# Kernel optimization log

Hardware: AMD Instinct MI355X
Metric: run time of the kernel (lower is better)

## Reference

```python
import math
import jax, jax.numpy as jnp
import numpy as np

B, S, H = 2, 2048, 1024
NH = 16
HD = H // NH            # 64
ROT = int(HD * 0.25)    # 16
QKV_SLOTS = 1024
PROJ_SLOTS = 1024
FFN_SLOTS = 4096
EPS = 1e-5


def gelu_l2_norm(x, axis=-1):
    # F.gelu (exact erf) then L2-normalize and rescale by sqrt(dim)
    g = jax.nn.gelu(x, approximate=False)
    n = jnp.linalg.norm(g, ord=2, axis=axis, keepdims=True)
    return g / n * math.sqrt(g.shape[axis])


def layer_norm(x, w, b):
    mu = jnp.mean(x, axis=-1, keepdims=True)
    var = jnp.mean(jnp.square(x - mu), axis=-1, keepdims=True)
    return (x - mu) * jax.lax.rsqrt(var + EPS) * w + b


def pattention(x, key_tok, val_tok):
    # [.., in] @ [slots, in]^T -> [.., slots]; NOTE: scale MULTIPLIES (as in source)
    aw = jnp.einsum('bsh,ph->bsp', x, key_tok) * math.sqrt(x.shape[-1])
    aw = gelu_l2_norm(aw, axis=-1)
    return jnp.einsum('bsp,pd->bsd', aw, val_tok)


def rotary_cos_sin(seq_len, rot_dim, base=10000.0):
    inv_freq = 1.0 / (base ** (jnp.arange(0, rot_dim, 2, dtype=jnp.float32) / rot_dim))
    t = jnp.arange(seq_len, dtype=jnp.float32)
    freqs = jnp.einsum('s,d->sd', t, inv_freq)           # [S, rot/2]
    emb = jnp.concatenate([freqs, freqs], axis=-1)       # [S, rot]
    return jnp.cos(emb), jnp.sin(emb)


def rotate_half(x):
    x1, x2 = jnp.split(x, 2, axis=-1)
    return jnp.concatenate([-x2, x1], axis=-1)


def setup_inputs() -> dict:
    key = jax.random.key(0)
    ks = jax.random.split(key, 12)
    p = lambda k, shape: jax.random.normal(k, shape, dtype=jnp.float32) * 0.02
    return {
        'x': jax.random.normal(ks[0], (B, S, H), dtype=jnp.float32),
        'ln1_w': jnp.ones((H,), jnp.float32), 'ln1_b': jnp.zeros((H,), jnp.float32),
        'ln2_w': jnp.ones((H,), jnp.float32), 'ln2_b': jnp.zeros((H,), jnp.float32),
        'q_key': p(ks[1], (QKV_SLOTS, H)), 'q_val': p(ks[2], (QKV_SLOTS, H)),
        'k_key': p(ks[3], (QKV_SLOTS, H)), 'k_val': p(ks[4], (QKV_SLOTS, H)),
        'v_key': p(ks[5], (QKV_SLOTS, H)), 'v_val': p(ks[6], (QKV_SLOTS, H)),
        'proj_key': p(ks[7], (PROJ_SLOTS, H)), 'proj_val': p(ks[8], (PROJ_SLOTS, H)),
        'ffn_key': p(ks[9], (FFN_SLOTS, H)), 'ffn_val': p(ks[10], (FFN_SLOTS, H)),
    }


def reference(x, ln1_w, ln1_b, ln2_w, ln2_b, q_key, q_val, k_key, k_val,
              v_key, v_val, proj_key, proj_val, ffn_key, ffn_val):
    residual = x
    xn = layer_norm(x, ln1_w, ln1_b)
    q = pattention(xn, q_key, q_val).reshape(B, S, NH, HD)
    k = pattention(xn, k_key, k_val).reshape(B, S, NH, HD)
    v = pattention(xn, v_key, v_val).reshape(B, S, NH, HD)

    cos, sin = rotary_cos_sin(S, ROT)          # [S, ROT]
    cos = cos[None, :, None, :]
    sin = sin[None, :, None, :]
    q_rot, q_pass = q[..., :ROT], q[..., ROT:]
    k_rot, k_pass = k[..., :ROT], k[..., ROT:]
    q_rot = q_rot * cos + rotate_half(q_rot) * sin
    k_rot = k_rot * cos + rotate_half(k_rot) * sin
    q = jnp.concatenate([q_rot, q_pass], axis=-1).transpose(0, 2, 1, 3)  # [B,NH,S,HD]
    k = jnp.concatenate([k_rot, k_pass], axis=-1).transpose(0, 2, 1, 3)
    v = v.transpose(0, 2, 1, 3)

    scale = math.sqrt(HD)
    causal = jnp.triu(jnp.ones((S, S), dtype=bool), k=1)
    attn_mask = jnp.where(causal, jnp.float32(-10000.0), jnp.float32(0.0))
    aw = jnp.einsum('bhqd,bhkd->bhqk', q, k) / scale + attn_mask
    aw = gelu_l2_norm(aw, axis=-1)
    o = jnp.einsum('bhqk,bhkd->bhqd', aw, v)
    o = o.transpose(0, 2, 1, 3).reshape(B, S, H)

    x = residual + pattention(o, proj_key, proj_val)
    residual = x
    x = residual + pattention(layer_norm(x, ln2_w, ln2_b), ffn_key, ffn_val)
    return x
```

## Files before the change

### kernel.cpp

```cpp
#include <hip/hip_runtime.h>

typedef __bf16 bf16x8 __attribute__((ext_vector_type(8)));
typedef float f32x4 __attribute__((ext_vector_type(4)));
typedef unsigned short u16;

__device__ __forceinline__ float b2f(u16 u) {
  union { unsigned int i; float f; } v; v.i = ((unsigned int)u) << 16; return v.f;
}
__device__ __forceinline__ u16 f2b(float f) {
  union { float f; unsigned int i; } v; v.f = f;
  unsigned int x = v.i;
  x += 0x7fffu + ((x >> 16) & 1u);
  return (u16)(x >> 16);
}
__device__ __forceinline__ float gelu_f(float x) {
  float x2 = x * x;
  float p = x * (1.5957691216f + 0.0713548162f * x2);
  float e = __expf(p);
  float r = __builtin_amdgcn_rcpf(1.0f + e);
  return x - x * r;
}
__device__ __forceinline__ void async16(const u16* g, u16* l) {
  __builtin_amdgcn_global_load_lds(
      (const __attribute__((address_space(1))) void*)g,
      (__attribute__((address_space(3))) void*)l, 16, 0, 0);
}
__device__ __forceinline__ void swz(int& bn, int& bm, int& bz) {
  int gx = (int)gridDim.x, gy = (int)gridDim.y;
  int flat = (int)(blockIdx.x + gridDim.x * (blockIdx.y + gridDim.y * blockIdx.z));
  int seq = flat >> 3;
  int nbm = gy >> 3;
  bm = (flat & 7) * nbm + seq % nbm;
  int rest = seq / nbm;
  bn = rest % gx;
  bz = rest / gx;
}

union U4 { uint4 u; u16 s[8]; };

__global__ __launch_bounds__(256) void cvt9_kernel(
    const float* __restrict__ qk, const float* __restrict__ kk,
    const float* __restrict__ vk, const float* __restrict__ pk,
    const float* __restrict__ fk, u16* __restrict__ w, float* __restrict__ ssqz) {
  int z = blockIdx.y;
  int i = blockIdx.x * 256 + threadIdx.x;
  if (z == 8) {
    if (i < 20480) ssqz[i] = 0.f;
    return;
  }
  const float* in = (z == 0) ? qk : (z == 1) ? kk : (z == 2) ? vk : (z == 3) ? pk
                    : fk + (size_t)(z - 4) * 1048576;
  u16* o = w + (size_t)z * 1048576;
  float4 f = ((const float4*)in)[i];
  ushort4 s;
  s.x = f2b(f.x); s.y = f2b(f.y); s.z = f2b(f.z); s.w = f2b(f.w);
  ((ushort4*)o)[i] = s;
}

__global__ __launch_bounds__(256) void cvtT8_kernel(
    const float* __restrict__ qv, const float* __restrict__ kv,
    const float* __restrict__ vv, const float* __restrict__ pv,
    const float* __restrict__ fv, u16* __restrict__ valsT, u16* __restrict__ fvT) {
  __shared__ float t[32][33];
  int z = blockIdx.z;
  const float* in; u16* o; int Rout, rowoff;
  if (z < 4) {
    in = (z == 0) ? qv : (z == 1) ? kv : (z == 2) ? vv : pv;
    o = valsT + (size_t)z * 1048576; Rout = 1024; rowoff = 0;
  } else {
    in = fv + (size_t)(z - 4) * 1048576;
    o = fvT; Rout = 4096; rowoff = (z - 4) * 1024;
  }
  int bc = blockIdx.x, br = blockIdx.y;
  int tid = threadIdx.x;
  int r = tid >> 5, cc = tid & 31;
  #pragma unroll
  for (int i = 0; i < 4; ++i)
    t[r + i * 8][cc] = in[(size_t)(br * 32 + r + i * 8) * 1024 + bc * 32 + cc];
  __syncthreads();
  #pragma unroll
  for (int i = 0; i < 4; ++i)
    o[(size_t)(bc * 32 + r + i * 8) * Rout + rowoff + br * 32 + cc] = f2b(t[cc][r + i * 8]);
}

__global__ __launch_bounds__(256) void ln_kernel(const float* __restrict__ x,
    const float* __restrict__ w, const float* __restrict__ b, u16* __restrict__ out) {
  int wv = threadIdx.x >> 6, lane = threadIdx.x & 63;
  int row = blockIdx.x * 4 + wv;
  const float* xr = x + (size_t)row * 1024;
  float4 v[4];
  float s = 0.f, s2 = 0.f;
  #pragma unroll
  for (int i = 0; i < 4; ++i) {
    v[i] = ((const float4*)xr)[lane + 64 * i];
    s += v[i].x + v[i].y + v[i].z + v[i].w;
    s2 += v[i].x * v[i].x + v[i].y * v[i].y + v[i].z * v[i].z + v[i].w * v[i].w;
  }
  #pragma unroll
  for (int m = 1; m < 64; m <<= 1) { s += __shfl_xor(s, m); s2 += __shfl_xor(s2, m); }
  float mu = s * (1.0f / 1024.0f);
  float inv = rsqrtf(s2 * (1.0f / 1024.0f) - mu * mu + 1e-5f);
  u16* orow = out + (size_t)row * 1024;
  #pragma unroll
  for (int i = 0; i < 4; ++i) {
    int c = (lane + 64 * i) * 4;
    ushort4 o;
    o.x = f2b((v[i].x - mu) * inv * w[c]     + b[c]);
    o.y = f2b((v[i].y - mu) * inv * w[c + 1] + b[c + 1]);
    o.z = f2b((v[i].z - mu) * inv * w[c + 2] + b[c + 2]);
    o.w = f2b((v[i].w - mu) * inv * w[c + 3] + b[c + 3]);
    ((ushort4*)orow)[lane + 64 * i] = o;
  }
}

__device__ __forceinline__ bf16x8 ldfrag(const u16* __restrict__ base, int row, int ks, int quad) {
  int off = (row * 64 + ks * 32 + quad * 8) ^ ((row & 7) << 3);
  return *(const bf16x8*)&base[off];
}

template <int EPI, bool ROT>
__global__ __launch_bounds__(512, 2) void gemm8(
    const u16* __restrict__ A, size_t sAz,
    const u16* __restrict__ B, size_t sBz,
    u16* __restrict__ C, size_t sCz,
    float* __restrict__ ssqb, size_t sSz,
    int N, int K, int kzs, int klen, float alpha) {
  __shared__ __align__(16) u16 As[2][2][8192];
  __shared__ __align__(16) u16 Bs[2][2][8192];
  int bn, bm, bz;
  swz(bn, bm, bz);
  int tid = threadIdx.x, lane = tid & 63, wv = tid >> 6;
  int quad = lane >> 4, l16 = lane & 15;
  int wm = wv >> 2, wn = wv & 3;
  const u16* Ab = A + (size_t)bz * sAz + (size_t)(bm * 256) * K;
  const u16* Bb = B + (size_t)bz * sBz + (size_t)(bn * 256) * K;
  int koff = bz * kzs;
  size_t off0, off1;
  {
    int r0 = wv * 16 + (lane >> 3);
    int r1 = r0 + 8;
    off0 = (size_t)r0 * K + ((lane & 7) ^ (r0 & 7)) * 8;
    off1 = (size_t)r1 * K + ((lane & 7) ^ (r1 & 7)) * 8;
  }
  int lds0 = wv * 1024, lds1 = wv * 1024 + 512;
  const size_t hK = (size_t)128 * K;
  auto STAGE = [&](const u16* gb, int k0, u16* lds) {
    async16(gb + off0 + k0, lds + lds0);
    async16(gb + off1 + k0, lds + lds1);
  };

  f32x4 zero = {0.f, 0.f, 0.f, 0.f};
  f32x4 acc[8][4];
  #pragma unroll
  for (int i = 0; i < 8; ++i)
    #pragma unroll
    for (int j = 0; j < 4; ++j) acc[i][j] = zero;

  int NT = klen >> 6;
  STAGE(Bb,      koff,      &Bs[0][0][0]);
  STAGE(Bb + hK, koff,      &Bs[0][1][0]);
  STAGE(Ab,      koff,      &As[0][0][0]);
  STAGE(Ab + hK, koff,      &As[0][1][0]);
  STAGE(Bb,      koff + 64, &Bs[1][0][0]);
  STAGE(Bb + hK, koff + 64, &Bs[1][1][0]);
  STAGE(Ab,      koff + 64, &As[1][0][0]);
  asm volatile("s_waitcnt vmcnt(6)" ::: "memory");
  __builtin_amdgcn_sched_barrier(0);
  __builtin_amdgcn_s_barrier();

  bf16x8 a[4][2], b[4][2];
  int brow = (wn & 1) * 64;
  for (int t = 0; t < NT; ++t) {
    int cur = t & 1;
    const u16* Ar = &As[cur][wm][0];
    const u16* Br = &Bs[cur][wn >> 1][0];
    #pragma unroll
    for (int j = 0; j < 4; ++j)
      #pragma unroll
      for (int ks = 0; ks < 2; ++ks)
        b[j][ks] = ldfrag(Br, brow + j * 16 + l16, ks, quad);
    #pragma unroll
    for (int i = 0; i < 4; ++i)
      #pragma unroll
      for (int ks = 0; ks < 2; ++ks)
        a[i][ks] = ldfrag(Ar, i * 16 + l16, ks, quad);
    if (t + 1 < NT) STAGE(Ab + hK, koff + (t + 1) * 64, &As[cur ^ 1][1][0]);
    __builtin_amdgcn_s_barrier();
    asm volatile("s_waitcnt lgkmcnt(0)" ::: "memory");
    __builtin_amdgcn_sched_barrier(0);
    __builtin_amdgcn_s_setprio(1);
    #pragma unroll
    for (int i = 0; i < 4; ++i)
      #pragma unroll
      for (int j = 0; j < 2; ++j) {
        acc[i][j] = __builtin_amdgcn_mfma_f32_16x16x32_bf16(a[i][0], b[j][0], acc[i][j], 0, 0, 0);
        acc[i][j] = __builtin_amdgcn_mfma_f32_16x16x32_bf16(a[i][1], b[j][1], acc[i][j], 0, 0, 0);
      }
    __builtin_amdgcn_s_setprio(0);
    __builtin_amdgcn_sched_barrier(0);
    __builtin_amdgcn_s_barrier();
    if (t + 2 < NT) STAGE(Bb, koff + (t + 2) * 64, &Bs[cur][0][0]);
    __builtin_amdgcn_s_barrier();
    __builtin_amdgcn_s_setprio(1);
    #pragma unroll
    for (int i = 0; i < 4; ++i)
      #pragma unroll
      for (int j = 2; j < 4; ++j) {
        acc[i][j] = __builtin_amdgcn_mfma_f32_16x16x32_bf16(a[i][0], b[j][0], acc[i][j], 0, 0, 0);
        acc[i][j] = __builtin_amdgcn_mfma_f32_16x16x32_bf16(a[i][1], b[j][1], acc[i][j], 0, 0, 0);
      }
    __builtin_amdgcn_s_setprio(0);
    __builtin_amdgcn_sched_barrier(0);
    __builtin_amdgcn_s_barrier();
    #pragma unroll
    for (int i = 0; i < 4; ++i)
      #pragma unroll
      for (int ks = 0; ks < 2; ++ks)
        a[i][ks] = ldfrag(Ar, 64 + i * 16 + l16, ks, quad);
    if (t + 2 < NT) STAGE(Bb + hK, koff + (t + 2) * 64, &Bs[cur][1][0]);
    __builtin_amdgcn_s_barrier();
    asm volatile("s_waitcnt lgkmcnt(0)" ::: "memory");
    __builtin_amdgcn_sched_barrier(0);
    __builtin_amdgcn_s_setprio(1);
    #pragma unroll
    for (int i = 0; i < 4; ++i)
      #pragma unroll
      for (int j = 0; j < 2; ++j) {
        acc[4 + i][j] = __builtin_amdgcn_mfma_f32_16x16x32_bf16(a[i][0], b[j][0], acc[4 + i][j], 0, 0, 0);
        acc[4 + i][j] = __builtin_amdgcn_mfma_f32_16x16x32_bf16(a[i][1], b[j][1], acc[4 + i][j], 0, 0, 0);
      }
    __builtin_amdgcn_s_setprio(0);
    __builtin_amdgcn_sched_barrier(0);
    __builtin_amdgcn_s_barrier();
    if (t + 2 < NT) STAGE(Ab, koff + (t + 2) * 64, &As[cur][0][0]);
    __builtin_amdgcn_s_barrier();
    __builtin_amdgcn_s_setprio(1);
    #pragma unroll
    for (int i = 0; i < 4; ++i)
      #pragma unroll
      for (int j = 2; j < 4; ++j) {
        acc[4 + i][j] = __builtin_amdgcn_mfma_f32_16x16x32_bf16(a[i][0], b[j][0], acc[4 + i][j], 0, 0, 0);
        acc[4 + i][j] = __builtin_amdgcn_mfma_f32_16x16x32_bf16(a[i][1], b[j][1], acc[4 + i][j], 0, 0, 0);
      }
    __builtin_amdgcn_s_setprio(0);
    if (t < NT - 1) {
      if (t == NT - 2) asm volatile("s_waitcnt vmcnt(0)" ::: "memory");
      else             asm volatile("s_waitcnt vmcnt(6)" ::: "memory");
    }
    __builtin_amdgcn_sched_barrier(0);
    __builtin_amdgcn_s_barrier();
  }

  #pragma unroll
  for (int i = 0; i < 8; ++i) {
    int rbase = bm * 256 + wm * 128 + i * 16 + quad * 4;
    if (EPI == 0) {
      float srow[4] = {0.f, 0.f, 0.f, 0.f};
      #pragma unroll
      for (int j = 0; j < 4; ++j) {
        int c = bn * 256 + wn * 64 + j * 16 + l16;
        #pragma unroll
        for (int reg = 0; reg < 4; ++reg) {
          float g = gelu_f(acc[i][j][reg] * alpha);
          srow[reg] += g * g;
          C[(size_t)bz * sCz + (size_t)(rbase + reg) * N + c] = f2b(g);
        }
      }
      #pragma unroll
      for (int reg = 0; reg < 4; ++reg) {
        float s = srow[reg];
        s += __shfl_xor(s, 1); s += __shfl_xor(s, 2);
        s += __shfl_xor(s, 4); s += __shfl_xor(s, 8);
        if (l16 == 0) atomicAdd(&ssqb[bz * sSz + rbase + reg], s);
      }
    } else if (EPI == 1) {
      float sc[4];
      #pragma unroll
      for (int reg = 0; reg < 4; ++reg)
        sc[reg] = alpha * rsqrtf(ssqb[bz * sSz + rbase + reg]);
      #pragma unroll
      for (int j = 0; j < 4; ++j) {
        int c = bn * 256 + wn * 64 + j * 16 + l16;
        #pragma unroll
        for (int reg = 0; reg < 4; ++reg) {
          float vs = acc[i][j][reg] * sc[reg];
          if (ROT && j == 0) {
            float prt = __shfl_xor(vs, 8);
            if (bz < 2) {
              int seq = (rbase + reg) & 2047;
              float fr = exp2f((float)(l16 & 7) * -1.66096404744368f);
              float ang = (float)seq * fr;
              float c_ = __cosf(ang), s_ = __sinf(ang);
              vs = (l16 < 8) ? (vs * c_ - prt * s_) : (vs * c_ + prt * s_);
            }
          }
          C[(size_t)bz * sCz + (size_t)(rbase + reg) * N + c] = f2b(vs);
        }
      }
    } else {
      float* Cf = (float*)C + (size_t)(bz >> 1) * sCz;
      #pragma unroll
      for (int j = 0; j < 4; ++j) {
        int c = bn * 256 + wn * 64 + j * 16 + l16;
        #pragma unroll
        for (int reg = 0; reg < 4; ++reg)
          atomicAdd(&Cf[(size_t)(rbase + reg) * N + c], acc[i][j][reg]);
      }
    }
  }
}

__global__ __launch_bounds__(256) void zz_kernel(float* __restrict__ p0,
                                                 float* __restrict__ p1) {
  size_t i = ((size_t)blockIdx.x * 256 + threadIdx.x) * 4;
  float4 z = {0.f, 0.f, 0.f, 0.f};
  *(float4*)(p0 + i) = z;
  *(float4*)(p1 + i) = z;
}

template <int TM>
__global__ __launch_bounds__(256) void gemm_key(
    const u16* __restrict__ A, size_t sAz,
    const u16* __restrict__ B, size_t sBz,
    u16* __restrict__ C, size_t sCz,
    float* __restrict__ ssqb, size_t sSz,
    int N, int K, float alpha) {
  constexpr int AI = TM / 32;
  __shared__ __align__(16) u16 As[2][TM * 32];
  __shared__ __align__(16) u16 Bs[2][128 * 32];
  int bn, bm, bz;
  swz(bn, bm, bz);
  const u16* Ab = A + (size_t)bz * sAz + (size_t)bm * TM * K;
  const u16* Bb = B + (size_t)bz * sBz + (size_t)bn * 128 * K;
  int tid = threadIdx.x, lane = tid & 63, wv = tid >> 6;
  int quad = lane >> 4, l16 = lane & 15;
  int lr = lane >> 2, lc = (lane & 3) * 8;
  int wm = wv >> 1, wn = wv & 1;
  int RB = wm * (TM / 2), CB = wn * 64;
  f32x4 zero = {0.f, 0.f, 0.f, 0.f};
  f32x4 acc[AI][4];
  #pragma unroll
  for (int i = 0; i < AI; ++i)
    #pragma unroll
    for (int j = 0; j < 4; ++j) acc[i][j] = zero;
  #pragma unroll
  for (int t = 0; t < TM / 64; ++t) {
    int ia = wv * (TM / 64) + t;
    async16(Ab + (size_t)(ia * 16 + lr) * K + lc, &As[0][ia * 512]);
  }
  #pragma unroll
  for (int t = 0; t < 2; ++t) {
    int ib = wv * 2 + t;
    async16(Bb + (size_t)(ib * 16 + lr) * K + lc, &Bs[0][ib * 512]);
  }
  for (int k0 = 0, cur = 0; k0 < K; k0 += 32, cur ^= 1) {
    __syncthreads();
    if (k0 + 32 < K) {
      #pragma unroll
      for (int t = 0; t < TM / 64; ++t) {
        int ia = wv * (TM / 64) + t;
        async16(Ab + (size_t)(ia * 16 + lr) * K + k0 + 32 + lc, &As[cur ^ 1][ia * 512]);
      }
      #pragma unroll
      for (int t = 0; t < 2; ++t) {
        int ib = wv * 2 + t;
        async16(Bb + (size_t)(ib * 16 + lr) * K + k0 + 32 + lc, &Bs[cur ^ 1][ib * 512]);
      }
    }
    bf16x8 af[AI], bf[4];
    #pragma unroll
    for (int i = 0; i < AI; ++i)
      af[i] = *(const bf16x8*)&As[cur][(RB + i * 16 + l16) * 32 + quad * 8];
    #pragma unroll
    for (int j = 0; j < 4; ++j)
      bf[j] = *(const bf16x8*)&Bs[cur][(CB + j * 16 + l16) * 32 + quad * 8];
    #pragma unroll
    for (int i = 0; i < AI; ++i)
      #pragma unroll
      for (int j = 0; j < 4; ++j)
        acc[i][j] = __builtin_amdgcn_mfma_f32_16x16x32_bf16(af[i], bf[j], acc[i][j], 0, 0, 0);
  }
  #pragma unroll
  for (int i = 0; i < AI; ++i) {
    int rbase = bm * TM + RB + i * 16 + quad * 4;
    float srow[4] = {0.f, 0.f, 0.f, 0.f};
    #pragma unroll
    for (int j = 0; j < 4; ++j) {
      int c = bn * 128 + CB + j * 16 + l16;
      #pragma unroll
      for (int reg = 0; reg < 4; ++reg) {
        float g = gelu_f(acc[i][j][reg] * alpha);
        srow[reg] += g * g;
        C[(size_t)bz * sCz + (size_t)(rbase + reg) * N + c] = f2b(g);
      }
    }
    #pragma unroll
    for (int reg = 0; reg < 4; ++reg) {
      float s = srow[reg];
      s += __shfl_xor(s, 1); s += __shfl_xor(s, 2);
      s += __shfl_xor(s, 4); s += __shfl_xor(s, 8);
      if (l16 == 0) atomicAdd(&ssqb[bz * sSz + rbase + reg], s);
    }
  }
}

template <int TM, int MODE, bool ROT>
__global__ __launch_bounds__(256) void gemm_val(
    const u16* __restrict__ A, size_t sAz,
    const u16* __restrict__ B, size_t sBz,
    void* __restrict__ C, size_t sCz,
    const float* __restrict__ ssqb, size_t sSz,
    int N, int K, int kzs, int klen, float sqrtP, const float* __restrict__ res) {
  constexpr int AI = TM / 32;
  __shared__ __align__(16) u16 As[2][TM * 32];
  __shared__ __align__(16) u16 Bs[2][128 * 32];
  int bn, bm, bz;
  swz(bn, bm, bz);
  const u16* Ab = A + (size_t)bz * sAz + (size_t)bm * TM * K;
  const u16* Bb = B + (size_t)bz * sBz + (size_t)bn * 128 * K;
  int tid = threadIdx.x, lane = tid & 63, wv = tid >> 6;
  int quad = lane >> 4, l16 = lane & 15;
  int lr = lane >> 2, lc = (lane & 3) * 8;
  int wm = wv >> 1, wn = wv & 1;
  int RB = wm * (TM / 2), CB = wn * 64;
  f32x4 zero = {0.f, 0.f, 0.f, 0.f};
  f32x4 acc[AI][4];
  #pragma unroll
  for (int i = 0; i < AI; ++i)
    #pragma unroll
    for (int j = 0; j < 4; ++j) acc[i][j] = zero;
  int kb0 = bz * kzs;
  #pragma unroll
  for (int t = 0; t < TM / 64; ++t) {
    int ia = wv * (TM / 64) + t;
    async16(Ab + (size_t)(ia * 16 + lr) * K + kb0 + lc, &As[0][ia * 512]);
  }
  #pragma unroll
  for (int t = 0; t < 2; ++t) {
    int ib = wv * 2 + t;
    async16(Bb + (size_t)(ib * 16 + lr) * K + kb0 + lc, &Bs[0][ib * 512]);
  }
  for (int k0 = kb0, cur = 0; k0 < kb0 + klen; k0 += 32, cur ^= 1) {
    __syncthreads();
    if (k0 + 32 < kb0 + klen) {
      #pragma unroll
      for (int t = 0; t < TM / 64; ++t) {
        int ia = wv * (TM / 64) + t;
        async16(Ab + (size_t)(ia * 16 + lr) * K + k0 + 32 + lc, &As[cur ^ 1][ia * 512]);
      }
      #pragma unroll
      for (int t = 0; t < 2; ++t) {
        int ib = wv * 2 + t;
        async16(Bb + (size_t)(ib * 16 + lr) * K + k0 + 32 + lc, &Bs[cur ^ 1][ib * 512]);
      }
    }
    bf16x8 af[AI], bf[4];
    #pragma unroll
    for (int i = 0; i < AI; ++i)
      af[i] = *(const bf16x8*)&As[cur][(RB + i * 16 + l16) * 32 + quad * 8];
    #pragma unroll
    for (int j = 0; j < 4; ++j)
      bf[j] = *(const bf16x8*)&Bs[cur][(CB + j * 16 + l16) * 32 + quad * 8];
    #pragma unroll
    for (int i = 0; i < AI; ++i)
      #pragma unroll
      for (int j = 0; j < 4; ++j)
        acc[i][j] = __builtin_amdgcn_mfma_f32_16x16x32_bf16(af[i], bf[j], acc[i][j], 0, 0, 0);
  }
  #pragma unroll
  for (int i = 0; i < AI; ++i) {
    int rbase = bm * TM + RB + i * 16 + quad * 4;
    float sc[4];
    if (MODE < 2) {
      #pragma unroll
      for (int reg = 0; reg < 4; ++reg)
        sc[reg] = sqrtP * rsqrtf(ssqb[bz * sSz + rbase + reg]);
    }
    #pragma unroll
    for (int j = 0; j < 4; ++j) {
      int c = bn * 128 + CB + j * 16 + l16;
      #pragma unroll
      for (int reg = 0; reg < 4; ++reg) {
        float v = acc[i][j][reg];
        size_t idx = (size_t)(rbase + reg) * N + c;
        if (MODE == 0) {
          ((u16*)C)[(size_t)bz * sCz + idx] = f2b(v * sc[reg]);
        } else if (MODE == 1) {
          ((float*)C)[idx] = v * sc[reg] + res[idx];
        } else {
          ((float*)C)[(size_t)bz * sCz + idx] = v;
        }
      }
    }
  }
}

__global__ __launch_bounds__(256) void vt_kernel(const u16* __restrict__ vb,
                                                 u16* __restrict__ vT) {
  __shared__ __align__(16) u16 T[64][72];
  int st = blockIdx.x, bh = blockIdx.y;
  int b = bh >> 4, h = bh & 15;
  int tid = threadIdx.x;
  #pragma unroll
  for (int i = 0; i < 2; ++i) {
    int l = tid + 256 * i;
    int s = l >> 3, dc = l & 7;
    *(uint4*)&T[s][dc * 8] =
        *(const uint4*)(vb + (size_t)(b * 2048 + st * 64 + s) * 1024 + h * 64 + dc * 8);
  }
  __syncthreads();
  #pragma unroll
  for (int i = 0; i < 2; ++i) {
    int l = tid + 256 * i;
    int d = l >> 3, scid = l & 7;
    int blk = (scid >> 2) * 32;
    int qq = (scid & 3) * 4;
    U4 u;
    #pragma unroll
    for (int j = 0; j < 8; ++j)
      u.s[j] = T[blk + (j >> 2) * 16 + qq + (j & 3)][d];
    *(uint4*)(vT + ((size_t)bh * 64 + d) * 2048 + st * 64 + scid * 8) = u.u;
  }
}

__global__ __launch_bounds__(256) void attn_kernel(
    const u16* __restrict__ qb, const u16* __restrict__ kb,
    const u16* __restrict__ vT, u16* __restrict__ ob) {
  __shared__ __align__(16) u16 Qs[64 * 64];
  __shared__ __align__(16) u16 Ks[2][64 * 64];
  __shared__ __align__(16) u16 Vts[2][64 * 64];
  int bh = blockIdx.x;
  int qt = 31 - (int)blockIdx.y;
  int b = bh >> 4, h = bh & 15;
  const u16* qp = qb + (size_t)b * 2048 * 1024 + h * 64;
  const u16* kp = kb + (size_t)b * 2048 * 1024 + h * 64;
  const u16* vp = vT + (size_t)bh * 64 * 2048;
  int tid = threadIdx.x, lane = tid & 63, wv = tid >> 6;
  int quad = lane >> 4, l16 = lane & 15;
  int lr8 = lane >> 3;
  int lc8s = ((lane & 7) ^ lr8) * 8;
  int rx = (l16 & 7) << 3;
  int MR = wv * 16;
  int nkt = qt + 1;
  #pragma unroll
  for (int t = 0; t < 2; ++t) {
    int idx = wv * 2 + t;
    async16(qp + (size_t)(qt * 64 + idx * 8 + lr8) * 1024 + lc8s, &Qs[idx * 512]);
    async16(kp + (size_t)(idx * 8 + lr8) * 1024 + lc8s, &Ks[0][idx * 512]);
    async16(vp + (size_t)(idx * 8 + lr8) * 2048 + lc8s, &Vts[0][idx * 512]);
  }
  f32x4 zero = {0.f, 0.f, 0.f, 0.f};
  f32x4 oacc[4];
  #pragma unroll
  for (int dn = 0; dn < 4; ++dn) oacc[dn] = zero;
  float ssql = 0.f;
  bf16x8 bq0 = {}, bq1 = {};
  for (int kt = 0, cur = 0; kt < nkt; ++kt, cur ^= 1) {
    __syncthreads();
    if (kt == 0) {
      bq0 = *(const bf16x8*)&Qs[((MR + l16) * 64 + quad * 8) ^ rx];
      bq1 = *(const bf16x8*)&Qs[((MR + l16) * 64 + 32 + quad * 8) ^ rx];
    }
    if (kt + 1 < nkt) {
      #pragma unroll
      for (int t = 0; t < 2; ++t) {
        int idx = wv * 2 + t;
        async16(kp + (size_t)((kt + 1) * 64 + idx * 8 + lr8) * 1024 + lc8s, &Ks[cur ^ 1][idx * 512]);
        async16(vp + (size_t)(idx * 8 + lr8) * 2048 + (kt + 1) * 64 + lc8s, &Vts[cur ^ 1][idx * 512]);
      }
    }
    bool dg = (kt == qt);
    #pragma unroll
    for (int kc = 0; kc < 2; ++kc) {
      bf16x8 pf;
      #pragma unroll
      for (int snh = 0; snh < 2; ++snh) {
        int sn = kc * 2 + snh;
        bf16x8 ak0 = *(const bf16x8*)&Ks[cur][((sn * 16 + l16) * 64 + quad * 8) ^ rx];
        bf16x8 ak1 = *(const bf16x8*)&Ks[cur][((sn * 16 + l16) * 64 + 32 + quad * 8) ^ rx];
        f32x4 st = zero;
        st = __builtin_amdgcn_mfma_f32_16x16x32_bf16(ak0, bq0, st, 0, 0, 0);
        st = __builtin_amdgcn_mfma_f32_16x16x32_bf16(ak1, bq1, st, 0, 0, 0);
        #pragma unroll
        for (int r = 0; r < 4; ++r) {
          float gl = gelu_f(st[r] * 0.125f);
          if (dg && (sn * 16 + quad * 4 + r > MR + l16)) gl = 0.f;
          ssql += gl * gl;
          pf[snh * 4 + r] = (__bf16)gl;
        }
      }
      #pragma unroll
      for (int dn = 0; dn < 4; ++dn) {
        bf16x8 bv = *(const bf16x8*)&Vts[cur][((dn * 16 + l16) * 64 + kc * 32 + quad * 8) ^ rx];
        oacc[dn] = __builtin_amdgcn_mfma_f32_16x16x32_bf16(pf, bv, oacc[dn], 0, 0, 0);
      }
    }
  }
  ssql += __shfl_xor(ssql, 16);
  ssql += __shfl_xor(ssql, 32);
  float sc = 45.254834f * rsqrtf(ssql);
  #pragma unroll
  for (int dn = 0; dn < 4; ++dn)
    #pragma unroll
    for (int r = 0; r < 4; ++r) {
      float scr = __shfl(sc, quad * 4 + r);
      int row = qt * 64 + MR + quad * 4 + r;
      int col = h * 64 + dn * 16 + l16;
      ob[(size_t)(b * 2048 + row) * 1024 + col] = f2b(oacc[dn][r] * scr);
    }
}

__global__ __launch_bounds__(256) void fin_kernel(
    const float* __restrict__ p0, const float* __restrict__ p1,
    const float* __restrict__ x1, const float* __restrict__ ssqf,
    float* __restrict__ out) {
  int row = blockIdx.x, t = threadIdx.x;
  float s = 64.0f * rsqrtf(ssqf[row]);
  size_t base = (size_t)row * 1024 + t * 4;
  float4 a = *(const float4*)(p0 + base);
  float4 b = *(const float4*)(p1 + base);
  float4 r = *(const float4*)(x1 + base);
  float4 o;
  o.x = r.x + s * (a.x + b.x); o.y = r.y + s * (a.y + b.y);
  o.z = r.z + s * (a.z + b.z); o.w = r.w + s * (a.w + b.w);
  *(float4*)(out + base) = o;
}

extern "C" void kernel_launch(void* const* d_in, const int* in_sizes, int n_in,
                              void* d_out, int out_size, void* d_ws, size_t ws_size,
                              hipStream_t stream) {
  const float* x    = (const float*)d_in[0];
  const float* ln1w = (const float*)d_in[1];
  const float* ln1b = (const float*)d_in[2];
  const float* ln2w = (const float*)d_in[3];
  const float* ln2b = (const float*)d_in[4];
  const float* qk   = (const float*)d_in[5];
  const float* qv   = (const float*)d_in[6];
  const float* kk   = (const float*)d_in[7];
  const float* kv   = (const float*)d_in[8];
  const float* vk   = (const float*)d_in[9];
  const float* vv   = (const float*)d_in[10];
  const float* pk   = (const float*)d_in[11];
  const float* pv   = (const float*)d_in[12];
  const float* fk   = (const float*)d_in[13];
  const float* fv   = (const float*)d_in[14];
  float* out = (float*)d_out;

  const size_t M1 = 1048576;
  u16* w = (u16*)d_ws;
  u16* wkeys  = w;
  u16* wpk    = w + 3 * M1;
  u16* wfk    = w + 4 * M1;
  u16* wvalsT = w + 8 * M1;
  u16* wpvT   = w + 11 * M1;
  u16* wfvT   = w + 12 * M1;
  u16* xn     = w + 16 * M1;
  u16* gq     = w + 20 * M1;
  u16* ob     = w + 20 * M1;
  u16* vT     = w + 24 * M1;
  u16* gp     = w + 28 * M1;
  u16* gf     = w + 20 * M1;
  u16* qb     = w + 36 * M1;
  u16* kb     = w + 40 * M1;
  u16* vb     = w + 44 * M1;
  float* ssq_qkv  = (float*)(w + 48 * M1);
  float* ssq_proj = ssq_qkv + 12288;
  float* ssq_ffn  = ssq_qkv + 16384;
  float* x1 = (float*)(w + 52 * M1);
  float* p0 = (float*)w;
  float* p1 = (float*)(w + 36 * M1);

  dim3 blk(256);
  cvt9_kernel<<<dim3(1024, 9), blk, 0, stream>>>(qk, kk, vk, pk, fk, w, ssq_qkv);
  cvtT8_kernel<<<dim3(32, 32, 8), blk, 0, stream>>>(qv, kv, vv, pv, fv, wvalsT, wfvT);

  ln_kernel<<<1024, blk, 0, stream>>>(x, ln1w, ln1b, xn);
  gemm8<0, false><<<dim3(4, 16, 3), 512, 0, stream>>>(
      xn, 0, wkeys, M1, gq, 4 * M1, ssq_qkv, 4096, 1024, 1024, 0, 1024, 32.0f);
  gemm8<1, true><<<dim3(4, 16, 3), 512, 0, stream>>>(
      gq, 4 * M1, wvalsT, M1, qb, 4 * M1, ssq_qkv, 4096, 1024, 1024, 0, 1024, 32.0f);

  vt_kernel<<<dim3(32, 32), blk, 0, stream>>>(vb, vT);
  attn_kernel<<<dim3(32, 32), blk, 0, stream>>>(qb, kb, vT, ob);

  gemm_key<64><<<dim3(8, 64, 1), blk, 0, stream>>>(
      ob, 0, wpk, 0, gp, 0, ssq_proj, 0, 1024, 1024, 32.0f);
  gemm_val<64, 1, false><<<dim3(8, 64, 1), blk, 0, stream>>>(
      gp, 0, wpvT, 0, x1, 0, ssq_proj, 0, 1024, 1024, 0, 1024, 32.0f, x);

  ln_kernel<<<1024, blk, 0, stream>>>(x1, ln2w, ln2b, xn);
  gemm8<0, false><<<dim3(16, 16, 1), 512, 0, stream>>>(
      xn, 0, wfk, 0, gf, 0, ssq_ffn, 0, 4096, 1024, 0, 1024, 32.0f);
  zz_kernel<<<4096, blk, 0, stream>>>(p0, p1);
  gemm8<2, false><<<dim3(4, 16, 4), 512, 0, stream>>>(
      gf, 0, wfvT, 0, (u16*)p0, 18 * M1, ssq_ffn, 0, 1024, 4096, 1024, 1024, 0.0f);
  fin_kernel<<<4096, blk, 0, stream>>>(p0, p1, x1, ssq_ffn, out);
}
```

Baseline: 476.6 us.

## Replace atomic split-K FFN reduction with plain partial stores and drop zeroing

```diff
diff --git a/kernel.cpp b/kernel.cpp
--- a/kernel.cpp
+++ b/kernel.cpp
@@ -135,6 +135,8 @@
   const u16* Ab = A + (size_t)bz * sAz + (size_t)(bm * 256) * K;
   const u16* Bb = B + (size_t)bz * sBz + (size_t)(bn * 256) * K;
   int koff = bz * kzs;
+  int kl = K - koff;
+  if (kl > klen) kl = klen;
   size_t off0, off1;
   {
     int r0 = wv * 16 + (lane >> 3);
@@ -156,7 +158,7 @@
     #pragma unroll
     for (int j = 0; j < 4; ++j) acc[i][j] = zero;
 
-  int NT = klen >> 6;
+  int NT = kl >> 6;
   STAGE(Bb,      koff,      &Bs[0][0][0]);
   STAGE(Bb + hK, koff,      &Bs[0][1][0]);
   STAGE(Ab,      koff,      &As[0][0][0]);
@@ -298,24 +300,17 @@
         }
       }
     } else {
-      float* Cf = (float*)C + (size_t)(bz >> 1) * sCz;
+      size_t zoff = (size_t)bz * 4194304 + (size_t)(bz >> 1) * 10485760;
+      float* Cf = (float*)C + zoff;
       #pragma unroll
       for (int j = 0; j < 4; ++j) {
         int c = bn * 256 + wn * 64 + j * 16 + l16;
         #pragma unroll
         for (int reg = 0; reg < 4; ++reg)
-          atomicAdd(&Cf[(size_t)(rbase + reg) * N + c], acc[i][j][reg]);
-      }
-    }
-  }
-}
-
-__global__ __launch_bounds__(256) void zz_kernel(float* __restrict__ p0,
-                                                 float* __restrict__ p1) {
-  size_t i = ((size_t)blockIdx.x * 256 + threadIdx.x) * 4;
-  float4 z = {0.f, 0.f, 0.f, 0.f};
-  *(float4*)(p0 + i) = z;
-  *(float4*)(p1 + i) = z;
+          Cf[(size_t)(rbase + reg) * N + c] = acc[i][j][reg];
+      }
+    }
+  }
 }
 
 template <int TM>
@@ -612,17 +607,18 @@
 
 __global__ __launch_bounds__(256) void fin_kernel(
     const float* __restrict__ p0, const float* __restrict__ p1,
-    const float* __restrict__ x1, const float* __restrict__ ssqf,
-    float* __restrict__ out) {
+    const float* __restrict__ p2, const float* __restrict__ x1,
+    const float* __restrict__ ssqf, float* __restrict__ out) {
   int row = blockIdx.x, t = threadIdx.x;
   float s = 64.0f * rsqrtf(ssqf[row]);
   size_t base = (size_t)row * 1024 + t * 4;
   float4 a = *(const float4*)(p0 + base);
   float4 b = *(const float4*)(p1 + base);
+  float4 c = *(const float4*)(p2 + base);
   float4 r = *(const float4*)(x1 + base);
   float4 o;
-  o.x = r.x + s * (a.x + b.x); o.y = r.y + s * (a.y + b.y);
-  o.z = r.z + s * (a.z + b.z); o.w = r.w + s * (a.w + b.w);
+  o.x = r.x + s * (a.x + b.x + c.x); o.y = r.y + s * (a.y + b.y + c.y);
+  o.z = r.z + s * (a.z + b.z + c.z); o.w = r.w + s * (a.w + b.w + c.w);
   *(float4*)(out + base) = o;
 }
 
@@ -653,8 +649,8 @@
   u16* wfk    = w + 4 * M1;
   u16* wvalsT = w + 8 * M1;
   u16* wpvT   = w + 11 * M1;
-  u16* wfvT   = w + 12 * M1;
-  u16* xn     = w + 16 * M1;
+  u16* xn     = w + 12 * M1;
+  u16* wfvT   = w + 16 * M1;
   u16* gq     = w + 20 * M1;
   u16* ob     = w + 20 * M1;
   u16* vT     = w + 24 * M1;
@@ -668,7 +664,8 @@
   float* ssq_ffn  = ssq_qkv + 16384;
   float* x1 = (float*)(w + 52 * M1);
   float* p0 = (float*)w;
-  float* p1 = (float*)(w + 36 * M1);
+  float* p1 = (float*)(w + 8 * M1);
+  float* p2 = (float*)(w + 36 * M1);
 
   dim3 blk(256);
   cvt9_kernel<<<dim3(1024, 9), blk, 0, stream>>>(qk, kk, vk, pk, fk, w, ssq_qkv);
@@ -691,8 +688,7 @@
   ln_kernel<<<1024, blk, 0, stream>>>(x1, ln2w, ln2b, xn);
   gemm8<0, false><<<dim3(16, 16, 1), 512, 0, stream>>>(
       xn, 0, wfk, 0, gf, 0, ssq_ffn, 0, 4096, 1024, 0, 1024, 32.0f);
-  zz_kernel<<<4096, blk, 0, stream>>>(p0, p1);
-  gemm8<2, false><<<dim3(4, 16, 4), 512, 0, stream>>>(
-      gf, 0, wfvT, 0, (u16*)p0, 18 * M1, ssq_ffn, 0, 1024, 4096, 1024, 1024, 0.0f);
-  fin_kernel<<<4096, blk, 0, stream>>>(p0, p1, x1, ssq_ffn, out);
-}
+  gemm8<2, false><<<dim3(4, 16, 3), 512, 0, stream>>>(
+      gf, 0, wfvT, 0, (u16*)p0, 0, ssq_ffn, 0, 1024, 4096, 1408, 1408, 0.0f);
+  fin_kernel<<<4096, blk, 0, stream>>>(p0, p1, p2, x1, ssq_ffn, out);
+}
```

After: 437.0 us. -8.3%, faster.
